# Kernel optimization log

Measured on AMD Instinct MI355X. Metric: run time of the kernel, lower is better.

Reference implementation:

```python
import jax, jax.numpy as jnp
import numpy as np
import math

HIDDEN = 2048
HEADS = 16
HEAD_DIM = HIDDEN // HEADS
MAX_SEQ = 4096
ROPE_BASE = 10000.0


def rope_cos_sin(seq_len):
    # (seq_len, head_dim//2) angle table
    inv_freq = 1.0 / (ROPE_BASE ** (jnp.arange(0, HEAD_DIM, 2, dtype=jnp.float32) / HEAD_DIM))
    t = jnp.arange(seq_len, dtype=jnp.float32)
    ang = jnp.einsum('s,f->sf', t, inv_freq)
    return jnp.cos(ang), jnp.sin(ang)


def apply_rope(x, cos, sin):
    # x: (b, s, h, d); interleaved complex pairs along last dim
    b, s, h, d = x.shape
    xr = x.reshape(b, s, h, d // 2, 2)
    x0, x1 = xr[..., 0], xr[..., 1]
    c = cos[:s][None, :, None, :]
    sn = sin[:s][None, :, None, :]
    o0 = x0 * c - x1 * sn
    o1 = x0 * sn + x1 * c
    return jnp.stack([o0, o1], axis=-1).reshape(b, s, h, d)


def setup_inputs() -> dict:
    key = jax.random.key(0)
    k1, k2, k3, k4, k5, k6 = jax.random.split(key, 6)
    B, SQ, SK = 2, 2048, 2048
    x = jax.random.normal(k1, (B, SQ, HIDDEN), dtype=jnp.float32)
    enc = jax.random.normal(k2, (B, SK, HIDDEN), dtype=jnp.float32)
    mask = jnp.ones((B, SK), dtype=jnp.int32)
    scale = 0.02
    Wq = jax.random.normal(k3, (HIDDEN, HIDDEN), dtype=jnp.float32) * scale
    Wk = jax.random.normal(k4, (HIDDEN, HIDDEN), dtype=jnp.float32) * scale
    Wv = jax.random.normal(k5, (HIDDEN, HIDDEN), dtype=jnp.float32) * scale
    Wo = jax.random.normal(k6, (HIDDEN, HIDDEN), dtype=jnp.float32) * scale
    return {"x": x, "encoder_output": enc, "encoder_attention_mask": mask,
            "Wq": Wq, "Wk": Wk, "Wv": Wv, "Wo": Wo}


def reference(x, encoder_output, encoder_attention_mask, Wq, Wk, Wv, Wo):
    B, SQ, _ = x.shape
    SK = encoder_output.shape[1]
    # nn.Linear(bias=False): y = x @ W^T
    q = (x @ Wq.T).reshape(B, SQ, HEADS, HEAD_DIM)
    k = (encoder_output @ Wk.T).reshape(B, SK, HEADS, HEAD_DIM)
    v = (encoder_output @ Wv.T).reshape(B, SK, HEADS, HEAD_DIM)
    cos, sin = rope_cos_sin(max(SQ, SK))
    q = apply_rope(q, cos, sin)
    k = apply_rope(k, cos, sin)
    scale = math.sqrt(HEAD_DIM)
    # (b, h, sq, sk) scores
    scores = jnp.einsum('bqhd,bkhd->bhqk', q, k) / scale
    mask = encoder_attention_mask[:, None, None, :]
    scores = jnp.where(mask == 0, -jnp.inf, scores)
    attn = jax.nn.softmax(scores, axis=-1)
    out = jnp.einsum('bhqk,bkhd->bqhd', attn, v).reshape(B, SQ, HIDDEN)
    return out @ Wo.T
```

## Files before the change

kernel.cpp:

```cpp
#include <hip/hip_runtime.h>
#include <stdint.h>


#define LOG2E 1.44269504088896340736f
#define INV2PI 0.15915494309189535f

typedef __attribute__((ext_vector_type(8))) short bf16x8;
typedef __attribute__((ext_vector_type(8))) uint16_t u16x8;
typedef __attribute__((ext_vector_type(4))) uint16_t u16x4;
typedef __attribute__((ext_vector_type(4))) float f32x4;

__device__ __forceinline__ uint16_t f2bf(float f) {
  union { float f; uint32_t i; } v; v.f = f;
  uint32_t x = v.i;
  return (uint16_t)((x + 0x7fffu + ((x >> 16) & 1u)) >> 16);
}
__device__ __forceinline__ uint32_t f_as_u(float f) { union { float f; uint32_t u; } v; v.f = f; return v.u; }
__device__ __forceinline__ float u_as_f(uint32_t u) { union { uint32_t u; float f; } v; v.u = u; return v.f; }
__device__ __forceinline__ void glds16(const void* g, void* l) {
  __builtin_amdgcn_global_load_lds((const __attribute__((address_space(1))) void*)g,
                                   (__attribute__((address_space(3))) void*)l, 16, 0, 0);
}

__global__ __launch_bounds__(256) void convert_xe(const float* __restrict__ x,
                                                  const float* __restrict__ enc,
                                                  uint16_t* __restrict__ xb,
                                                  uint16_t* __restrict__ encb) {
  const int blk = blockIdx.x;
  const float* src = (blk < 4096) ? x : enc;
  uint16_t* dst = (blk < 4096) ? xb : encb;
  const long off = ((long)(blk & 4095) * 256 + threadIdx.x) * 8;
  const f32x4 a = *(const f32x4*)(src + off);
  const f32x4 b = *(const f32x4*)(src + off + 4);
  u16x8 o;
#pragma unroll
  for (int j = 0; j < 4; ++j) { o[j] = f2bf(a[j]); o[4 + j] = f2bf(b[j]); }
  *(u16x8*)(dst + off) = o;
}

__global__ __launch_bounds__(256) void convert_w4(const float* __restrict__ Wq,
                                                  const float* __restrict__ Wk,
                                                  const float* __restrict__ Wv,
                                                  const float* __restrict__ Wo,
                                                  uint16_t* __restrict__ W4) {
  const int blk = blockIdx.x;
  const int sec = blk >> 11;
  const long off = ((long)(blk & 2047) * 256 + threadIdx.x) * 8;
  const float* src = (sec == 0) ? Wq : (sec == 1) ? Wk : (sec == 2) ? Wv : Wo;
  const f32x4 a = *(const f32x4*)(src + off);
  const f32x4 b = *(const f32x4*)(src + off + 4);
  u16x8 o;
#pragma unroll
  for (int j = 0; j < 4; ++j) { o[j] = f2bf(a[j]); o[4 + j] = f2bf(b[j]); }
  *(u16x8*)(W4 + (long)sec * 4194304 + off) = o;
}

__global__ __launch_bounds__(256) void mask_bias(const int* __restrict__ m,
                                                 float* __restrict__ bias) {
  const int i = blockIdx.x * 256 + threadIdx.x;
  bias[i] = m[i] ? 0.0f : -__builtin_inff();
}

__device__ __forceinline__ void epi_rope_store(uint16_t* C, const f32x4& a, int rowbase,
                                               int c, float oscale) {
  const int f = (c >> 1) & 63;
  const float inv = __builtin_amdgcn_exp2f((float)f * (-13.287712379549449f / 64.0f));
  const float sgn = (c & 1) ? 1.0f : -1.0f;
#pragma unroll
  for (int r = 0; r < 4; ++r) {
    const float val = a[r];
    const float partner = __shfl_xor(val, 1);
    const int s = (rowbase + r) & 2047;
    const float rev = __builtin_amdgcn_fractf((float)s * inv * INV2PI);
    const float sn = __builtin_amdgcn_sinf(rev);
    const float cs = __builtin_amdgcn_cosf(rev);
    C[(long)(rowbase + r) * 2048 + c] = f2bf((val * cs + sgn * partner * sn) * oscale);
  }
}

__global__ __launch_bounds__(512, 2) void gemm256(const uint16_t* __restrict__ A0,
                                                  const uint16_t* __restrict__ A1,
                                                  const uint16_t* __restrict__ W,
                                                  uint16_t* __restrict__ Qb,
                                                  uint16_t* __restrict__ Kb,
                                                  uint16_t* __restrict__ Vtb,
                                                  int M, int N, int K, float oscale) {
  __shared__ __align__(16) uint16_t As[2][2][8192];
  __shared__ __align__(16) uint16_t Bs[2][2][8192];
  const int tid = threadIdx.x;
  const int lane = tid & 63;
  const int w = tid >> 6;
  const int r16 = lane & 15, quad = lane >> 4;
  const int wm = w >> 2, wn = w & 3;

  const int nby = M >> 8;
  const int nwg = gridDim.x;
  const int wg = ((int)blockIdx.x & 7) * (nwg >> 3) + ((int)blockIdx.x >> 3);
  const int by = wg % nby, bx = wg / nby;
  const int m0 = by << 8, n0 = bx << 8;

  const uint16_t* A = (n0 >= 2048) ? A1 : A0;

  const int srow = 2 * w * 16 + (lane >> 2);
  const int ssl = (lane & 3) ^ ((srow >> 1) & 3);
  const uint16_t* Ag0 = A + (long)(m0 + srow) * K + ssl * 8;
  const uint16_t* Ag1 = Ag0 + (long)16 * K;
  const uint16_t* Bg0 = W + (long)(n0 + srow) * K + ssl * 8;
  const uint16_t* Bg1 = Bg0 + (long)16 * K;
  const int ldso = w << 10;

  const int sw = (r16 >> 1) & 3;
  const int aoff = (wm * 128 + r16) * 32 + ((quad ^ sw) << 3);
  const int boff = (wn * 64 + r16) * 32 + ((quad ^ sw) << 3);

  f32x4 acc[8][4] = {};
  bf16x8 af[4], bfr[4];

#define SCHED0() __builtin_amdgcn_sched_barrier(0)
#define G_STAGE_A(BUF, KK, T) do { \
    glds16(Ag0 + (long)(T) * 64 + (KK) * 32, &As[BUF][KK][ldso]); \
    glds16(Ag1 + (long)(T) * 64 + (KK) * 32, &As[BUF][KK][ldso + 512]); } while (0)
#define G_STAGE_B(BUF, KK, T) do { \
    glds16(Bg0 + (long)(T) * 64 + (KK) * 32, &Bs[BUF][KK][ldso]); \
    glds16(Bg1 + (long)(T) * 64 + (KK) * 32, &Bs[BUF][KK][ldso + 512]); } while (0)
#define LDS_B(BUF, KK) do { _Pragma("unroll") \
    for (int i = 0; i < 4; ++i) bfr[i] = *(const bf16x8*)&Bs[BUF][KK][boff + i * 512]; } while (0)
#define LDS_A(BUF, KK, MH) do { _Pragma("unroll") \
    for (int i = 0; i < 4; ++i) af[i] = *(const bf16x8*)&As[BUF][KK][aoff + ((MH) * 4 + i) * 512]; } while (0)
#define MFMA16(MH) do { __builtin_amdgcn_s_setprio(1); _Pragma("unroll") \
    for (int mi = 0; mi < 4; ++mi) { _Pragma("unroll") \
      for (int nt = 0; nt < 4; ++nt) \
        acc[(MH) * 4 + mi][nt] = __builtin_amdgcn_mfma_f32_16x16x32_bf16(af[mi], bfr[nt], acc[(MH) * 4 + mi][nt], 0, 0, 0); } \
    __builtin_amdgcn_s_setprio(0); } while (0)
#define VMBAR(NN) do { SCHED0(); \
    asm volatile("s_waitcnt vmcnt(" #NN ")" ::: "memory"); \
    __builtin_amdgcn_s_barrier(); \
    SCHED0(); } while (0)
#define TILE_ITER(T, BC, BN) do { \
    G_STAGE_A(BN, 0, (T) + 1); LDS_B(BC, 0); LDS_A(BC, 0, 0); MFMA16(0); \
    G_STAGE_B(BN, 0, (T) + 1); LDS_A(BC, 0, 1); MFMA16(1); \
    VMBAR(4); \
    G_STAGE_A(BN, 1, (T) + 1); LDS_B(BC, 1); LDS_A(BC, 1, 0); MFMA16(0); \
    G_STAGE_B(BN, 1, (T) + 1); LDS_A(BC, 1, 1); MFMA16(1); \
    VMBAR(4); } while (0)

  G_STAGE_A(0, 0, 0); G_STAGE_B(0, 0, 0); G_STAGE_A(0, 1, 0); G_STAGE_B(0, 1, 0);
  VMBAR(4);

  const int NT = K >> 6;
  int t = 0;
  for (; t + 2 < NT; t += 2) { TILE_ITER(t, 0, 1); TILE_ITER(t + 1, 1, 0); }
  TILE_ITER(t, 0, 1);

  LDS_B(1, 0); LDS_A(1, 0, 0); MFMA16(0);
  LDS_A(1, 0, 1); MFMA16(1);
  VMBAR(0);
  LDS_B(1, 1); LDS_A(1, 1, 0); MFMA16(0);
  LDS_A(1, 1, 1); MFMA16(1);

#undef G_STAGE_A
#undef G_STAGE_B
#undef LDS_A
#undef LDS_B
#undef MFMA16
#undef TILE_ITER
#undef VMBAR
#undef SCHED0

#pragma unroll
  for (int mt = 0; mt < 8; ++mt)
#pragma unroll
    for (int nt = 0; nt < 4; ++nt) {
      const int col = n0 + wn * 64 + nt * 16 + r16;
      const int rowbase = m0 + wm * 128 + mt * 16 + quad * 4;
      if (n0 < 2048) {
        epi_rope_store(Qb, acc[mt][nt], rowbase, col, oscale);
      } else if (n0 < 4096) {
        epi_rope_store(Kb, acc[mt][nt], rowbase, col - 2048, 1.0f);
      } else {
        const int c = col - 4096;
        const int h = c >> 7, d = c & 127;
        const int b = rowbase >> 11, s = rowbase & 2047;
        u16x4 pk;
#pragma unroll
        for (int r = 0; r < 4; ++r) pk[r] = f2bf(acc[mt][nt][r]);
        *(u16x4*)(Vtb + (long)((b * 16 + h) * 128 + d) * 2048 + s) = pk;
      }
    }
}

__global__ __launch_bounds__(256) void gemm_proj64(const uint16_t* __restrict__ A,
                                                   const uint16_t* __restrict__ W,
                                                   float* __restrict__ C,
                                                   int M, int N, int K) {
  __shared__ __align__(16) uint16_t As[2][64 * 32];
  __shared__ __align__(16) uint16_t Bs[2][128 * 32];
  const int tid = threadIdx.x;
  const int lane = tid & 63;
  const int w = tid >> 6;
  const int r16 = lane & 15, quad = lane >> 4;
  const int m0 = blockIdx.y * 64, n0 = blockIdx.x * 128;
  const int wm = w >> 1, wn = w & 1;
  f32x4 acc[2][4] = {};
  const int scol = (lane & 3) * 8;
  const uint16_t* Ag  = A + (long)(m0 + 16 * w + (lane >> 2)) * K + scol;
  const uint16_t* Bg0 = W + (long)(n0 + 32 * w + (lane >> 2)) * K + scol;
  const uint16_t* Bg1 = Bg0 + (long)16 * K;

  glds16(Ag, &As[0][w * 512]);
  glds16(Bg0, &Bs[0][2 * w * 512]);
  glds16(Bg1, &Bs[0][2 * w * 512 + 512]);

  auto body = [&](int k1, const uint16_t* Ac, const uint16_t* Bc,
                  uint16_t* An, uint16_t* Bn, bool pf) {
    __syncthreads();
    if (pf) {
      glds16(Ag + k1, An + w * 512);
      glds16(Bg0 + k1, Bn + 2 * w * 512);
      glds16(Bg1 + k1, Bn + 2 * w * 512 + 512);
    }
    bf16x8 af[2], bfr[4];
#pragma unroll
    for (int mt = 0; mt < 2; ++mt)
      af[mt] = *(const bf16x8*)(Ac + (wm * 32 + mt * 16 + r16) * 32 + quad * 8);
#pragma unroll
    for (int nt = 0; nt < 4; ++nt)
      bfr[nt] = *(const bf16x8*)(Bc + (wn * 64 + nt * 16 + r16) * 32 + quad * 8);
#pragma unroll
    for (int mt = 0; mt < 2; ++mt)
#pragma unroll
      for (int nt = 0; nt < 4; ++nt)
        acc[mt][nt] = __builtin_amdgcn_mfma_f32_16x16x32_bf16(af[mt], bfr[nt], acc[mt][nt], 0, 0, 0);
  };

  const int NK2 = K >> 6;
  for (int kk = 0; kk < NK2; ++kk) {
    body((2 * kk + 1) * 32, &As[0][0], &Bs[0][0], &As[1][0], &Bs[1][0], true);
    body((2 * kk + 2) * 32, &As[1][0], &Bs[1][0], &As[0][0], &Bs[0][0], kk < NK2 - 1);
  }

#pragma unroll
  for (int mt = 0; mt < 2; ++mt)
#pragma unroll
    for (int nt = 0; nt < 4; ++nt) {
      const int col = n0 + wn * 64 + nt * 16 + r16;
      const int rowbase = m0 + wm * 32 + mt * 16 + quad * 4;
#pragma unroll
      for (int r = 0; r < 4; ++r)
        C[(long)(rowbase + r) * N + col] = acc[mt][nt][r];
    }
}

__global__ __launch_bounds__(512, 4) void attn_kernel(const uint16_t* __restrict__ Q,
                                                      const uint16_t* __restrict__ K,
                                                      const uint16_t* __restrict__ Vt,
                                                      const float* __restrict__ bias,
                                                      uint16_t* __restrict__ O) {
  __shared__ __align__(16) uint16_t Ks[2][32 * 128];
  __shared__ __align__(16) uint16_t Vts[2][128 * 32];
  __shared__ __align__(16) uint16_t Ps[8][16 * 40];
  const int tid = threadIdx.x;
  const int lane = tid & 63;
  const int w = tid >> 6;
  const int r16 = lane & 15, quad = lane >> 4;
  const int h = blockIdx.y, b = blockIdx.z;
  const int qbase = blockIdx.x * 128 + w * 16;

  bf16x8 qf[4];
  {
    const uint16_t* qb = Q + ((long)(b * 2048 + qbase + r16)) * 2048 + h * 128 + quad * 8;
#pragma unroll
    for (int c = 0; c < 4; ++c) qf[c] = *(const bf16x8*)(qb + c * 32);
  }
  f32x4 oacc[8] = {};
  float li[4] = {};

  uint16_t* PsW = &Ps[w][0];
  const float* brow = bias + b * 2048;

  const int kkey = 4 * w + quad;
  const uint16_t* kg = K + ((long)(b * 2048 + kkey)) * 2048 + h * 128
                         + 8 * (r16 ^ (kkey & 7));
  const int vdim = 16 * w + (lane >> 2);
  const uint16_t* vg = Vt + ((long)((b * 16 + h) * 128 + vdim)) * 2048
                          + 8 * ((lane & 3) ^ ((lane >> 2) & 3));

  glds16(kg, &Ks[0][w * 512]);
  glds16(vg, &Vts[0][w * 512]);
  kg += 32 * 2048;
  vg += 32;
  float bn0 = brow[r16], bn1 = brow[16 + r16];

  auto body = [&](int k0, const uint16_t* Kc, const uint16_t* Vc,
                  uint16_t* Kn, uint16_t* Vn, bool pf) {
    __syncthreads();
    const float bc0 = bn0, bc1 = bn1;
    if (pf) {
      glds16(kg, Kn + w * 512);
      glds16(vg, Vn + w * 512);
      kg += 32 * 2048;
      vg += 32;
      bn0 = brow[k0 + 32 + r16];
      bn1 = brow[k0 + 48 + r16];
    }
#pragma unroll
    for (int ct = 0; ct < 2; ++ct) {
      const int key = ct * 16 + r16;
      const int kb = key & 7;
      bf16x8 kf[4];
#pragma unroll
      for (int c = 0; c < 4; ++c)
        kf[c] = *(const bf16x8*)(Kc + key * 128 + ((4 * c + quad) ^ kb) * 8);
      const float bv = ct ? bc1 : bc0;
      const int pc = ct * 2 + (r16 >> 3);
      f32x4 s = {};
#pragma unroll
      for (int c = 0; c < 4; ++c)
        s = __builtin_amdgcn_mfma_f32_16x16x32_bf16(qf[c], kf[c], s, 0, 0, 0);
#pragma unroll
      for (int r = 0; r < 4; ++r) {
        const float p = __builtin_amdgcn_exp2f(s[r] + bv);
        const uint32_t pb = f_as_u(p) + 0x8000u;
        const int row = quad * 4 + r;
        PsW[row * 40 + ((pc ^ quad) << 3) + (r16 & 7)] = (uint16_t)(pb >> 16);
        li[r] += u_as_f(pb & 0xffff0000u);
      }
    }
    bf16x8 pa = *(const bf16x8*)(PsW + r16 * 40 + ((quad ^ (r16 >> 2)) << 3));
#pragma unroll
    for (int nt = 0; nt < 8; ++nt) {
      const int dim = nt * 16 + r16;
      bf16x8 vf = *(const bf16x8*)(Vc + dim * 32 + ((quad ^ (dim & 3)) << 3));
      oacc[nt] = __builtin_amdgcn_mfma_f32_16x16x32_bf16(pa, vf, oacc[nt], 0, 0, 0);
    }
  };

  for (int kt2 = 0; kt2 < 32; ++kt2) {
    body(64 * kt2,      &Ks[0][0], &Vts[0][0], &Ks[1][0], &Vts[1][0], true);
    body(64 * kt2 + 32, &Ks[1][0], &Vts[1][0], &Ks[0][0], &Vts[0][0], kt2 < 31);
  }

#pragma unroll
  for (int off = 1; off < 16; off <<= 1)
#pragma unroll
    for (int r = 0; r < 4; ++r) li[r] += __shfl_xor(li[r], off);

  uint16_t* ob = O + ((long)(b * 2048 + qbase)) * 2048 + h * 128;
  float inv_l[4];
#pragma unroll
  for (int r = 0; r < 4; ++r) inv_l[r] = 1.0f / li[r];
#pragma unroll
  for (int nt = 0; nt < 8; ++nt)
#pragma unroll
    for (int r = 0; r < 4; ++r)
      ob[(long)(quad * 4 + r) * 2048 + nt * 16 + r16] = f2bf(oacc[nt][r] * inv_l[r]);
}

extern "C" void kernel_launch(void* const* d_in, const int* in_sizes, int n_in,
                              void* d_out, int out_size, void* d_ws, size_t ws_size,
                              hipStream_t stream) {
  const float* x   = (const float*)d_in[0];
  const float* enc = (const float*)d_in[1];
  const int*   msk = (const int*)d_in[2];
  const float* Wq  = (const float*)d_in[3];
  const float* Wk  = (const float*)d_in[4];
  const float* Wv  = (const float*)d_in[5];
  const float* Wo  = (const float*)d_in[6];
  float* out = (float*)d_out;

  const long NELT = 8L * 1024 * 1024;
  const long WELT = 4L * 1024 * 1024;
  uint16_t* Qb  = (uint16_t*)d_ws;
  uint16_t* Kb  = Qb + NELT;
  uint16_t* Vtb = Kb + NELT;
  uint16_t* W4  = Vtb + NELT;
  float* biasb  = (float*)(W4 + 4 * WELT);
  uint16_t* xb   = (uint16_t*)d_out;
  uint16_t* encb = xb + NELT;
  uint16_t* Ob   = W4;

  const float cs_exp = 0.088388347648318447f * LOG2E;

  convert_xe<<<8192, 256, 0, stream>>>(x, enc, xb, encb);
  convert_w4<<<8192, 256, 0, stream>>>(Wq, Wk, Wv, Wo, W4);
  mask_bias<<<16, 256, 0, stream>>>(msk, biasb);

  gemm256<<<384, 512, 0, stream>>>(xb, encb, W4, Qb, Kb, Vtb,
                                   4096, 6144, 2048, cs_exp);

  attn_kernel<<<dim3(16, 16, 2), 512, 0, stream>>>(Qb, Kb, Vtb, biasb, Ob);

  gemm_proj64<<<dim3(16, 64), 256, 0, stream>>>(Ob, W4 + 3 * WELT, out,
                                                4096, 2048, 2048);
}
```

Measured before the change: 452.9 us.

## Triple-buffer attention K/V loads and fuse prep conversion kernels

Merges the three preprocessing kernels (activation conversion, weight conversion, mask bias) into one launch. The attention loop moves from double to triple buffering of K/V tiles in LDS, with an explicit vmcnt wait so two tile loads stay in flight. The aim is to cut launch overhead and hide global-load latency behind the MFMA work. The cost is more LDS per block, which may lower occupancy at 4 blocks per CU.

```diff
diff --git a/kernel.cpp b/kernel.cpp
--- a/kernel.cpp
+++ b/kernel.cpp
@@ -22,43 +22,43 @@
                                    (__attribute__((address_space(3))) void*)l, 16, 0, 0);
 }
 
-__global__ __launch_bounds__(256) void convert_xe(const float* __restrict__ x,
-                                                  const float* __restrict__ enc,
-                                                  uint16_t* __restrict__ xb,
-                                                  uint16_t* __restrict__ encb) {
+__global__ __launch_bounds__(256) void prep(const float* __restrict__ x,
+                                            const float* __restrict__ enc,
+                                            const float* __restrict__ Wq,
+                                            const float* __restrict__ Wk,
+                                            const float* __restrict__ Wv,
+                                            const float* __restrict__ Wo,
+                                            const int* __restrict__ msk,
+                                            uint16_t* __restrict__ xb,
+                                            uint16_t* __restrict__ encb,
+                                            uint16_t* __restrict__ W4,
+                                            float* __restrict__ bias) {
   const int blk = blockIdx.x;
-  const float* src = (blk < 4096) ? x : enc;
-  uint16_t* dst = (blk < 4096) ? xb : encb;
-  const long off = ((long)(blk & 4095) * 256 + threadIdx.x) * 8;
-  const f32x4 a = *(const f32x4*)(src + off);
-  const f32x4 b = *(const f32x4*)(src + off + 4);
-  u16x8 o;
-#pragma unroll
-  for (int j = 0; j < 4; ++j) { o[j] = f2bf(a[j]); o[4 + j] = f2bf(b[j]); }
-  *(u16x8*)(dst + off) = o;
-}
-
-__global__ __launch_bounds__(256) void convert_w4(const float* __restrict__ Wq,
-                                                  const float* __restrict__ Wk,
-                                                  const float* __restrict__ Wv,
-                                                  const float* __restrict__ Wo,
-                                                  uint16_t* __restrict__ W4) {
-  const int blk = blockIdx.x;
-  const int sec = blk >> 11;
-  const long off = ((long)(blk & 2047) * 256 + threadIdx.x) * 8;
-  const float* src = (sec == 0) ? Wq : (sec == 1) ? Wk : (sec == 2) ? Wv : Wo;
-  const f32x4 a = *(const f32x4*)(src + off);
-  const f32x4 b = *(const f32x4*)(src + off + 4);
-  u16x8 o;
-#pragma unroll
-  for (int j = 0; j < 4; ++j) { o[j] = f2bf(a[j]); o[4 + j] = f2bf(b[j]); }
-  *(u16x8*)(W4 + (long)sec * 4194304 + off) = o;
-}
-
-__global__ __launch_bounds__(256) void mask_bias(const int* __restrict__ m,
-                                                 float* __restrict__ bias) {
-  const int i = blockIdx.x * 256 + threadIdx.x;
-  bias[i] = m[i] ? 0.0f : -__builtin_inff();
+  if (blk < 16384) {
+    const float* src;
+    uint16_t* dst;
+    long off;
+    if (blk < 8192) {
+      src = (blk < 4096) ? x : enc;
+      dst = (blk < 4096) ? xb : encb;
+      off = ((long)(blk & 4095) * 256 + threadIdx.x) * 8;
+    } else {
+      const int wblk = blk - 8192;
+      const int sec = wblk >> 11;
+      src = (sec == 0) ? Wq : (sec == 1) ? Wk : (sec == 2) ? Wv : Wo;
+      dst = W4 + (long)sec * 4194304;
+      off = ((long)(wblk & 2047) * 256 + threadIdx.x) * 8;
+    }
+    const f32x4 a = *(const f32x4*)(src + off);
+    const f32x4 b = *(const f32x4*)(src + off + 4);
+    u16x8 o;
+#pragma unroll
+    for (int j = 0; j < 4; ++j) { o[j] = f2bf(a[j]); o[4 + j] = f2bf(b[j]); }
+    *(u16x8*)(dst + off) = o;
+  } else {
+    const int i = (blk - 16384) * 256 + threadIdx.x;
+    bias[i] = msk[i] ? 0.0f : -__builtin_inff();
+  }
 }
 
 __device__ __forceinline__ void epi_rope_store(uint16_t* C, const f32x4& a, int rowbase,
@@ -164,8 +164,6 @@
 #undef LDS_B
 #undef MFMA16
 #undef TILE_ITER
-#undef VMBAR
-#undef SCHED0
 
 #pragma unroll
   for (int mt = 0; mt < 8; ++mt)
@@ -256,8 +254,8 @@
                                                       const uint16_t* __restrict__ Vt,
                                                       const float* __restrict__ bias,
                                                       uint16_t* __restrict__ O) {
-  __shared__ __align__(16) uint16_t Ks[2][32 * 128];
-  __shared__ __align__(16) uint16_t Vts[2][128 * 32];
+  __shared__ __align__(16) uint16_t Ks[3][32 * 128];
+  __shared__ __align__(16) uint16_t Vts[3][128 * 32];
   __shared__ __align__(16) uint16_t Ps[8][16 * 40];
   const int tid = threadIdx.x;
   const int lane = tid & 63;
@@ -285,24 +283,34 @@
   const uint16_t* vg = Vt + ((long)((b * 16 + h) * 128 + vdim)) * 2048
                           + 8 * ((lane & 3) ^ ((lane >> 2) & 3));
 
+  float bn0 = brow[r16], bn1 = brow[16 + r16];
   glds16(kg, &Ks[0][w * 512]);
   glds16(vg, &Vts[0][w * 512]);
-  kg += 32 * 2048;
-  vg += 32;
-  float bn0 = brow[r16], bn1 = brow[16 + r16];
-
-  auto body = [&](int k0, const uint16_t* Kc, const uint16_t* Vc,
-                  uint16_t* Kn, uint16_t* Vn, bool pf) {
-    __syncthreads();
+  kg += 32 * 2048; vg += 32;
+  glds16(kg, &Ks[1][w * 512]);
+  glds16(vg, &Vts[1][w * 512]);
+  kg += 32 * 2048; vg += 32;
+
+  int cur = 0;
+  for (int j = 0; j < 64; ++j) {
+    __builtin_amdgcn_sched_barrier(0);
+    asm volatile("s_waitcnt vmcnt(2)" ::: "memory");
+    __builtin_amdgcn_s_barrier();
+    __builtin_amdgcn_sched_barrier(0);
     const float bc0 = bn0, bc1 = bn1;
-    if (pf) {
-      glds16(kg, Kn + w * 512);
-      glds16(vg, Vn + w * 512);
-      kg += 32 * 2048;
-      vg += 32;
-      bn0 = brow[k0 + 32 + r16];
-      bn1 = brow[k0 + 48 + r16];
-    }
+    if (j < 63) {
+      bn0 = brow[(j + 1) * 32 + r16];
+      bn1 = brow[(j + 1) * 32 + 16 + r16];
+    }
+    if (j < 62) {
+      const int nxt = (cur >= 1) ? cur - 1 : 2;
+      glds16(kg, &Ks[nxt][w * 512]);
+      glds16(vg, &Vts[nxt][w * 512]);
+      kg += 32 * 2048; vg += 32;
+    }
+    const uint16_t* Kc = &Ks[cur][0];
+    const uint16_t* Vc = &Vts[cur][0];
+
 #pragma unroll
     for (int ct = 0; ct < 2; ++ct) {
       const int key = ct * 16 + r16;
@@ -333,11 +341,7 @@
       bf16x8 vf = *(const bf16x8*)(Vc + dim * 32 + ((quad ^ (dim & 3)) << 3));
       oacc[nt] = __builtin_amdgcn_mfma_f32_16x16x32_bf16(pa, vf, oacc[nt], 0, 0, 0);
     }
-  };
-
-  for (int kt2 = 0; kt2 < 32; ++kt2) {
-    body(64 * kt2,      &Ks[0][0], &Vts[0][0], &Ks[1][0], &Vts[1][0], true);
-    body(64 * kt2 + 32, &Ks[1][0], &Vts[1][0], &Ks[0][0], &Vts[0][0], kt2 < 31);
+    cur = (cur >= 2) ? 0 : cur + 1;
   }
 
 #pragma unroll
@@ -381,9 +385,7 @@
 
   const float cs_exp = 0.088388347648318447f * LOG2E;
 
-  convert_xe<<<8192, 256, 0, stream>>>(x, enc, xb, encb);
-  convert_w4<<<8192, 256, 0, stream>>>(Wq, Wk, Wv, Wo, W4);
-  mask_bias<<<16, 256, 0, stream>>>(msk, biasb);
+  prep<<<16400, 256, 0, stream>>>(x, enc, Wq, Wk, Wv, Wo, msk, xb, encb, W4, biasb);
 
   gemm256<<<384, 512, 0, stream>>>(xb, encb, W4, Qb, Kb, Vtb,
                                    4096, 6144, 2048, cs_exp);
```

Result: no change. 450.9 us (-0.4%).
